# Performance work log

Measured on AMD Instinct MI355X. Metric: run time of the kernel, lower is better.

Reference implementation:

```python
import jax, jax.numpy as jnp
import numpy as np

S, N, D, F, E = 2048, 8, 1024, 4096, 8
STD = 0.02


def setup_inputs() -> dict:
    key = jax.random.key(0)
    ks = jax.random.split(key, 5)
    x = jax.random.normal(ks[0], (S, N, D), dtype=jnp.float32)
    Wg = jax.random.normal(ks[1], (E, D), dtype=jnp.float32) * STD
    W1 = jax.random.normal(ks[2], (E, F, D), dtype=jnp.float32) * STD
    b1 = jnp.zeros((E, F), dtype=jnp.float32)
    W2 = jax.random.normal(ks[3], (E, D, F), dtype=jnp.float32) * STD
    b2 = jnp.zeros((E, D), dtype=jnp.float32)
    return {"x": x, "Wg": Wg, "W1": W1, "b1": b1, "W2": W2, "b2": b2}


def reference(x, Wg, W1, b1, W2, b2):
    # Gate (eval mode: no gating noise). scores: [S, N, E]
    scores = jnp.einsum('snd,ed->sne', x, Wg)
    prob = jax.nn.softmax(scores, axis=-1)
    top1_idx = jnp.argmax(prob, axis=-1)                                   # [S, N] int
    top1_prob = jnp.take_along_axis(prob, top1_idx[..., None], axis=-1)[..., 0]  # [S, N]

    y = jnp.zeros_like(x)
    n_experts = Wg.shape[0]
    for e in range(n_experts):  # small fixed loop over experts
        h = jax.nn.gelu(jnp.einsum('snd,fd->snf', x, W1[e]) + b1[e], approximate=False)
        ye = jnp.einsum('snf,df->snd', h, W2[e]) + b2[e]
        mask = (top1_idx == e)[..., None]                                  # [S, N, 1]
        y = y + jnp.where(mask, ye * top1_prob[..., None], 0.0)
    return y
```

## Files before the change

kernel.cpp:

```cpp
#include <hip/hip_runtime.h>

#define S_TOK 16384
#define D_DIM 1024
#define F_DIM 4096
#define E_NUM 8

#define BM 128
#define BN 128
#define BK 32
#define MT_MAX 136

typedef short bf16x8 __attribute__((ext_vector_type(8)));
typedef float f32x4 __attribute__((ext_vector_type(4)));
typedef unsigned short ushort_t;

static __device__ __forceinline__ unsigned short f32_bf16(float f) {
  unsigned u = __float_as_uint(f);
  return (unsigned short)((u + 0x7FFFu + ((u >> 16) & 1u)) >> 16);
}

static __device__ __forceinline__ unsigned int pack_bf16x2(float a, float b) {
  unsigned ua = __float_as_uint(a);
  unsigned ub = __float_as_uint(b);
  unsigned lo = (ua + 0x7FFFu + ((ua >> 16) & 1u)) >> 16;
  unsigned hi = (ub + 0x7FFFu + ((ub >> 16) & 1u)) & 0xFFFF0000u;
  return lo | hi;
}

static __device__ __forceinline__ uint2 cvt_f4_bf4(const float4 v) {
  uint2 r;
  r.x = pack_bf16x2(v.x, v.y);
  r.y = pack_bf16x2(v.z, v.w);
  return r;
}

static __device__ __forceinline__ void load_lds16(const void* g, void* l) {
  __builtin_amdgcn_global_load_lds(g, l, 16, 0, 0);
}

__global__ void zero_counts_kernel(int* counts) {
  if (threadIdx.x < E_NUM) counts[threadIdx.x] = 0;
}

__global__ void cast2_kernel(const float* __restrict__ w1, ushort_t* __restrict__ o1,
                             const float* __restrict__ w2, ushort_t* __restrict__ o2) {
  const int half = 16384;
  const float* src = (blockIdx.x < half) ? w1 : w2;
  ushort_t* dst = (blockIdx.x < half) ? o1 : o2;
  const int b = (blockIdx.x < half) ? blockIdx.x : (blockIdx.x - half);
  const size_t base = ((size_t)b * blockDim.x + threadIdx.x) * 8;
  const float4 v0 = *(const float4*)(src + base);
  const float4 v1 = *(const float4*)(src + base + 4);
  const uint2 a = cvt_f4_bf4(v0), c = cvt_f4_bf4(v1);
  uint4 w; w.x = a.x; w.y = a.y; w.z = c.x; w.w = c.y;
  *(uint4*)(dst + base) = w;
}

__global__ void gate_kernel(const float* __restrict__ x,
                            const float* __restrict__ Wg,
                            ushort_t* __restrict__ xbf,
                            float* __restrict__ prob,
                            int* __restrict__ counts,
                            int* __restrict__ tok_list) {
  const int wv = threadIdx.x >> 6;
  const int lane = threadIdx.x & 63;
  const int t = blockIdx.x * 4 + wv;
  const float* xr = x + (size_t)t * D_DIM;
  ushort_t* xb = xbf + (size_t)t * D_DIM;

  float acc[E_NUM];
#pragma unroll
  for (int e = 0; e < E_NUM; ++e) acc[e] = 0.0f;

#pragma unroll
  for (int i = 0; i < 4; ++i) {
    const int k = i * 256 + lane * 4;
    const float4 v = *(const float4*)(xr + k);
    *(uint2*)(xb + k) = cvt_f4_bf4(v);
#pragma unroll
    for (int e = 0; e < E_NUM; ++e) {
      const float4 w = *(const float4*)(Wg + e * D_DIM + k);
      acc[e] += v.x * w.x + v.y * w.y + v.z * w.z + v.w * w.w;
    }
  }
#pragma unroll
  for (int e = 0; e < E_NUM; ++e) {
#pragma unroll
    for (int off = 32; off > 0; off >>= 1)
      acc[e] += __shfl_xor(acc[e], off, 64);
  }
  if (lane == 0) {
    float m = acc[0]; int bi = 0;
#pragma unroll
    for (int e = 1; e < E_NUM; ++e) {
      if (acc[e] > m) { m = acc[e]; bi = e; }
    }
    float s = 0.0f;
#pragma unroll
    for (int e = 0; e < E_NUM; ++e) s += expf(acc[e] - m);
    prob[t] = 1.0f / s;
    int p = atomicAdd(&counts[bi], 1);
    tok_list[bi * S_TOK + p] = t;
  }
}

__global__ void plan_kernel(const int* __restrict__ counts, int* __restrict__ plan) {
  if (threadIdx.x == 0) {
    int t = 0;
    for (int e = 0; e < E_NUM; ++e) {
      const int nt = (counts[e] + BM - 1) / BM;
      for (int i = 0; i < nt; ++i) {
        plan[1 + t] = e;
        plan[1 + MT_MAX + t] = i * BM;
        ++t;
      }
    }
    plan[0] = t;
  }
}

template <int KDIM, int NDIM, int EPI>
__launch_bounds__(256, 4)
__global__ void ffn_kernel(const ushort_t* __restrict__ A,
                           const ushort_t* __restrict__ B,
                           const float* __restrict__ bias,
                           const float* __restrict__ prob,
                           const int* __restrict__ counts,
                           const int* __restrict__ tok_list,
                           const int* __restrict__ plan,
                           ushort_t* __restrict__ Hout,
                           float* __restrict__ out) {
  constexpr int NT = NDIM / BN;
  constexpr int NK = KDIM / BK;
  const int ntiles = plan[0];
  const int live = ntiles * NT;
  if (blockIdx.x >= live) return;
  const int q = live >> 3, r = live & 7;
  const int xcd = blockIdx.x & 7, idx = blockIdx.x >> 3;
  const int wg = (xcd < r ? xcd * (q + 1) : r * (q + 1) + (xcd - r) * q) + idx;
  const int tile = wg / NT;
  const int n0 = (wg % NT) * BN;
  const int e = plan[1 + tile];
  const int m0 = plan[1 + MT_MAX + tile];
  const int cnt = counts[e];

  __shared__ ushort_t As[2][BM * BK];
  __shared__ ushort_t Bs[2][BM * BK];

  const int tid = threadIdx.x;
  const int lane = tid & 63;
  const int w = tid >> 6;
  const int wr = (w >> 1) * 64;
  const int wc = (w & 1) * 64;
  const int l15 = lane & 15;
  const int l4  = lane >> 4;

  const int srow = tid >> 2;
  const int sslot = ((tid & 3) ^ ((srow >> 1) & 3)) * 8;
  const int dstoff = w * 512;

  const size_t ebase = (size_t)e * S_TOK;
  const int tokA0 = (m0 + srow < cnt) ? tok_list[ebase + m0 + srow] : 0;
  const int tokA1 = (m0 + 64 + srow < cnt) ? tok_list[ebase + m0 + 64 + srow] : 0;
  const ushort_t* pA0 = A + (size_t)tokA0 * KDIM + sslot;
  const ushort_t* pA1 = A + (size_t)tokA1 * KDIM + sslot;
  const ushort_t* Be = B + (size_t)e * NDIM * KDIM;
  const ushort_t* pB0 = Be + (size_t)(n0 + srow) * KDIM + sslot;
  const ushort_t* pB1 = Be + (size_t)(n0 + 64 + srow) * KDIM + sslot;

  int oA[4], oB[4];
#pragma unroll
  for (int m = 0; m < 4; ++m) {
    const int rr = wr + m * 16 + l15;
    oA[m] = rr * BK + ((l4 ^ ((rr >> 1) & 3)) * 8);
  }
#pragma unroll
  for (int n = 0; n < 4; ++n) {
    const int rr = wc + n * 16 + l15;
    oB[n] = rr * BK + ((l4 ^ ((rr >> 1) & 3)) * 8);
  }

  f32x4 acc[4][4];
#pragma unroll
  for (int i = 0; i < 4; ++i)
#pragma unroll
    for (int j = 0; j < 4; ++j)
      acc[i][j] = (f32x4){0.f, 0.f, 0.f, 0.f};

  load_lds16(pA0, &As[0][dstoff]);
  load_lds16(pA1, &As[0][2048 + dstoff]);
  load_lds16(pB0, &Bs[0][dstoff]);
  load_lds16(pB1, &Bs[0][2048 + dstoff]);
  __syncthreads();

  int cb = 0;
  for (int t = 0; t < NK; ++t) {
    if (t + 1 < NK) {
      const int k0 = (t + 1) * BK;
      const int nb = cb ^ 1;
      load_lds16(pA0 + k0, &As[nb][dstoff]);
      load_lds16(pA1 + k0, &As[nb][2048 + dstoff]);
      load_lds16(pB0 + k0, &Bs[nb][dstoff]);
      load_lds16(pB1 + k0, &Bs[nb][2048 + dstoff]);
    }

    bf16x8 a[4], b[4];
#pragma unroll
    for (int i = 0; i < 4; ++i) {
      a[i] = *(const bf16x8*)&As[cb][oA[i]];
      b[i] = *(const bf16x8*)&Bs[cb][oB[i]];
    }
#pragma unroll
    for (int mi = 0; mi < 4; ++mi)
#pragma unroll
      for (int ni = 0; ni < 4; ++ni)
        acc[mi][ni] = __builtin_amdgcn_mfma_f32_16x16x32_bf16(a[mi], b[ni], acc[mi][ni], 0, 0, 0);

    __syncthreads();
    cb ^= 1;
  }

  const float* be = bias + (size_t)e * NDIM;
#pragma unroll
  for (int mi = 0; mi < 4; ++mi) {
#pragma unroll
    for (int rr = 0; rr < 4; ++rr) {
      const int slot = m0 + wr + mi * 16 + l4 * 4 + rr;
      if (slot >= cnt) continue;
      const int tok = tok_list[ebase + slot];
      if (EPI == 0) {
        ushort_t* hrow = Hout + (size_t)tok * NDIM;
#pragma unroll
        for (int ni = 0; ni < 4; ++ni) {
          const int col = n0 + wc + ni * 16 + l15;
          float v = acc[mi][ni][rr] + be[col];
          v = 0.5f * v * (1.0f + erff(v * 0.70710678118654752f));
          hrow[col] = f32_bf16(v);
        }
      } else {
        const float p = prob[tok];
        float* orow = out + (size_t)tok * NDIM;
#pragma unroll
        for (int ni = 0; ni < 4; ++ni) {
          const int col = n0 + wc + ni * 16 + l15;
          orow[col] = (acc[mi][ni][rr] + be[col]) * p;
        }
      }
    }
  }
}

extern "C" void kernel_launch(void* const* d_in, const int* in_sizes, int n_in,
                              void* d_out, int out_size, void* d_ws, size_t ws_size,
                              hipStream_t stream) {
  const float* x  = (const float*)d_in[0];
  const float* Wg = (const float*)d_in[1];
  const float* W1 = (const float*)d_in[2];
  const float* b1 = (const float*)d_in[3];
  const float* W2 = (const float*)d_in[4];
  const float* b2 = (const float*)d_in[5];
  float* out = (float*)d_out;

  const size_t MB = 1ull << 20;
  char* ws = (char*)d_ws;
  int* counts      = (int*)(ws);
  int* plan        = (int*)(ws + 4096);
  float* prob      = (float*)(ws + 64 * 1024);
  int* tok_list    = (int*)(ws + 128 * 1024);
  ushort_t* xbf    = (ushort_t*)(ws + 1 * MB);
  ushort_t* W1bf   = (ushort_t*)(ws + 33 * MB);
  ushort_t* W2bf   = (ushort_t*)(ws + 97 * MB);
  ushort_t* H      = (ushort_t*)(ws + 161 * MB);

  zero_counts_kernel<<<1, 64, 0, stream>>>(counts);
  gate_kernel<<<S_TOK / 4, 256, 0, stream>>>(x, Wg, xbf, prob, counts, tok_list);
  plan_kernel<<<1, 64, 0, stream>>>(counts, plan);

  cast2_kernel<<<32768, 256, 0, stream>>>(W1, W1bf, W2, W2bf);

  ffn_kernel<D_DIM, F_DIM, 0><<<(F_DIM / BN) * MT_MAX, 256, 0, stream>>>(
      xbf, W1bf, b1, nullptr, counts, tok_list, plan, H, nullptr);

  ffn_kernel<F_DIM, D_DIM, 1><<<(D_DIM / BN) * MT_MAX, 256, 0, stream>>>(
      H, W2bf, b2, prob, counts, tok_list, plan, nullptr, out);
}
```

Measured before the change: 761.2 us.

## Double K tile to 64 and drop LDS double buffering in grouped MoE GEMM

Result: faster. 709.3 us (-6.8%).

```diff
diff --git a/kernel.cpp b/kernel.cpp
--- a/kernel.cpp
+++ b/kernel.cpp
@@ -7,7 +7,7 @@
 
 #define BM 128
 #define BN 128
-#define BK 32
+#define BK 64
 #define MT_MAX 136
 
 typedef short bf16x8 __attribute__((ext_vector_type(8)));
@@ -144,8 +144,8 @@
   const int m0 = plan[1 + MT_MAX + tile];
   const int cnt = counts[e];
 
-  __shared__ ushort_t As[2][BM * BK];
-  __shared__ ushort_t Bs[2][BM * BK];
+  __shared__ ushort_t As[BM * BK];
+  __shared__ ushort_t Bs[BM * BK];
 
   const int tid = threadIdx.x;
   const int lane = tid & 63;
@@ -155,29 +155,36 @@
   const int l15 = lane & 15;
   const int l4  = lane >> 4;
 
-  const int srow = tid >> 2;
-  const int sslot = ((tid & 3) ^ ((srow >> 1) & 3)) * 8;
-  const int dstoff = w * 512;
+  const int sub = lane >> 3;
+  const int sslot = ((lane & 7) ^ sub) * 8;
+  const int dstoff = w * 2048;
 
   const size_t ebase = (size_t)e * S_TOK;
-  const int tokA0 = (m0 + srow < cnt) ? tok_list[ebase + m0 + srow] : 0;
-  const int tokA1 = (m0 + 64 + srow < cnt) ? tok_list[ebase + m0 + 64 + srow] : 0;
-  const ushort_t* pA0 = A + (size_t)tokA0 * KDIM + sslot;
-  const ushort_t* pA1 = A + (size_t)tokA1 * KDIM + sslot;
   const ushort_t* Be = B + (size_t)e * NDIM * KDIM;
-  const ushort_t* pB0 = Be + (size_t)(n0 + srow) * KDIM + sslot;
-  const ushort_t* pB1 = Be + (size_t)(n0 + 64 + srow) * KDIM + sslot;
-
-  int oA[4], oB[4];
+  const ushort_t* pA[4];
+  const ushort_t* pB[4];
+#pragma unroll
+  for (int j = 0; j < 4; ++j) {
+    const int ra = m0 + w * 32 + j * 8 + sub;
+    const int tok = (ra < cnt) ? tok_list[ebase + ra] : 0;
+    pA[j] = A + (size_t)tok * KDIM + sslot;
+    pB[j] = Be + (size_t)(n0 + w * 32 + j * 8 + sub) * KDIM + sslot;
+  }
+
+  int oA[4][2], oB[4][2];
 #pragma unroll
   for (int m = 0; m < 4; ++m) {
     const int rr = wr + m * 16 + l15;
-    oA[m] = rr * BK + ((l4 ^ ((rr >> 1) & 3)) * 8);
+#pragma unroll
+    for (int kk = 0; kk < 2; ++kk)
+      oA[m][kk] = rr * BK + (((kk * 4 + l4) ^ (rr & 7)) * 8);
   }
 #pragma unroll
   for (int n = 0; n < 4; ++n) {
     const int rr = wc + n * 16 + l15;
-    oB[n] = rr * BK + ((l4 ^ ((rr >> 1) & 3)) * 8);
+#pragma unroll
+    for (int kk = 0; kk < 2; ++kk)
+      oB[n][kk] = rr * BK + (((kk * 4 + l4) ^ (rr & 7)) * 8);
   }
 
   f32x4 acc[4][4];
@@ -187,37 +194,31 @@
     for (int j = 0; j < 4; ++j)
       acc[i][j] = (f32x4){0.f, 0.f, 0.f, 0.f};
 
-  load_lds16(pA0, &As[0][dstoff]);
-  load_lds16(pA1, &As[0][2048 + dstoff]);
-  load_lds16(pB0, &Bs[0][dstoff]);
-  load_lds16(pB1, &Bs[0][2048 + dstoff]);
-  __syncthreads();
-
-  int cb = 0;
   for (int t = 0; t < NK; ++t) {
-    if (t + 1 < NK) {
-      const int k0 = (t + 1) * BK;
-      const int nb = cb ^ 1;
-      load_lds16(pA0 + k0, &As[nb][dstoff]);
-      load_lds16(pA1 + k0, &As[nb][2048 + dstoff]);
-      load_lds16(pB0 + k0, &Bs[nb][dstoff]);
-      load_lds16(pB1 + k0, &Bs[nb][2048 + dstoff]);
-    }
-
-    bf16x8 a[4], b[4];
-#pragma unroll
-    for (int i = 0; i < 4; ++i) {
-      a[i] = *(const bf16x8*)&As[cb][oA[i]];
-      b[i] = *(const bf16x8*)&Bs[cb][oB[i]];
-    }
-#pragma unroll
-    for (int mi = 0; mi < 4; ++mi)
-#pragma unroll
-      for (int ni = 0; ni < 4; ++ni)
-        acc[mi][ni] = __builtin_amdgcn_mfma_f32_16x16x32_bf16(a[mi], b[ni], acc[mi][ni], 0, 0, 0);
-
+    const int k0 = t * BK;
+#pragma unroll
+    for (int j = 0; j < 4; ++j) {
+      load_lds16(pA[j] + k0, &As[dstoff + j * 512]);
+      load_lds16(pB[j] + k0, &Bs[dstoff + j * 512]);
+    }
     __syncthreads();
-    cb ^= 1;
+
+#pragma unroll
+    for (int kk = 0; kk < 2; ++kk) {
+      bf16x8 a[4], b[4];
+#pragma unroll
+      for (int i = 0; i < 4; ++i) {
+        a[i] = *(const bf16x8*)&As[oA[i][kk]];
+        b[i] = *(const bf16x8*)&Bs[oB[i][kk]];
+      }
+#pragma unroll
+      for (int mi = 0; mi < 4; ++mi)
+#pragma unroll
+        for (int ni = 0; ni < 4; ++ni)
+          acc[mi][ni] = __builtin_amdgcn_mfma_f32_16x16x32_bf16(a[mi], b[ni], acc[mi][ni], 0, 0, 0);
+    }
+
+    __syncthreads();
   }
 
   const float* be = bias + (size_t)e * NDIM;
```

## Triple-buffer LDS loads with explicit vmcnt waits and reorder tile mapping

Applied to the files above, without the earlier changes.

Result: slower. 790.8 us (+3.9%).

```diff
diff --git a/kernel.cpp b/kernel.cpp
--- a/kernel.cpp
+++ b/kernel.cpp
@@ -36,6 +36,16 @@
 
 static __device__ __forceinline__ void load_lds16(const void* g, void* l) {
   __builtin_amdgcn_global_load_lds(g, l, 16, 0, 0);
+}
+
+static __device__ __forceinline__ float gelu_f(float v) {
+  const float u = fabsf(v) * 0.70710678118654752f;
+  const float t = 1.0f / (1.0f + 0.3275911f * u);
+  const float poly = t * (0.254829592f + t * (-0.284496736f + t * (1.421413741f +
+                     t * (-1.453152027f + t * 1.061405429f))));
+  const float erfa = 1.0f - poly * __expf(-u * u);
+  const float erfv = (v >= 0.0f) ? erfa : -erfa;
+  return 0.5f * v * (1.0f + erfv);
 }
 
 __global__ void zero_counts_kernel(int* counts) {
@@ -119,8 +129,10 @@
   }
 }
 
+#define SWZ(r) ((((r) & 3) ^ (((r) >> 2) & 3)))
+
 template <int KDIM, int NDIM, int EPI>
-__launch_bounds__(256, 4)
+__launch_bounds__(256, 3)
 __global__ void ffn_kernel(const ushort_t* __restrict__ A,
                            const ushort_t* __restrict__ B,
                            const float* __restrict__ bias,
@@ -138,14 +150,14 @@
   const int q = live >> 3, r = live & 7;
   const int xcd = blockIdx.x & 7, idx = blockIdx.x >> 3;
   const int wg = (xcd < r ? xcd * (q + 1) : r * (q + 1) + (xcd - r) * q) + idx;
-  const int tile = wg / NT;
-  const int n0 = (wg % NT) * BN;
+  const int tile = wg % ntiles;
+  const int n0 = (wg / ntiles) * BN;
   const int e = plan[1 + tile];
   const int m0 = plan[1 + MT_MAX + tile];
   const int cnt = counts[e];
 
-  __shared__ ushort_t As[2][BM * BK];
-  __shared__ ushort_t Bs[2][BM * BK];
+  __shared__ ushort_t As[3][BM * BK];
+  __shared__ ushort_t Bs[3][BM * BK];
 
   const int tid = threadIdx.x;
   const int lane = tid & 63;
@@ -156,8 +168,8 @@
   const int l4  = lane >> 4;
 
   const int srow = tid >> 2;
-  const int sslot = ((tid & 3) ^ ((srow >> 1) & 3)) * 8;
-  const int dstoff = w * 512;
+  const int sslot = ((tid & 3) ^ SWZ(srow)) * 8;
+  const int w512 = w * 512;
 
   const size_t ebase = (size_t)e * S_TOK;
   const int tokA0 = (m0 + srow < cnt) ? tok_list[ebase + m0 + srow] : 0;
@@ -172,12 +184,12 @@
 #pragma unroll
   for (int m = 0; m < 4; ++m) {
     const int rr = wr + m * 16 + l15;
-    oA[m] = rr * BK + ((l4 ^ ((rr >> 1) & 3)) * 8);
+    oA[m] = rr * BK + ((l4 ^ SWZ(rr)) * 8);
   }
 #pragma unroll
   for (int n = 0; n < 4; ++n) {
     const int rr = wc + n * 16 + l15;
-    oB[n] = rr * BK + ((l4 ^ ((rr >> 1) & 3)) * 8);
+    oB[n] = rr * BK + ((l4 ^ SWZ(rr)) * 8);
   }
 
   f32x4 acc[4][4];
@@ -187,22 +199,20 @@
     for (int j = 0; j < 4; ++j)
       acc[i][j] = (f32x4){0.f, 0.f, 0.f, 0.f};
 
-  load_lds16(pA0, &As[0][dstoff]);
-  load_lds16(pA1, &As[0][2048 + dstoff]);
-  load_lds16(pB0, &Bs[0][dstoff]);
-  load_lds16(pB1, &Bs[0][2048 + dstoff]);
-  __syncthreads();
+#pragma unroll
+  for (int p = 0; p < 3; ++p) {
+    const int k0 = p * BK;
+    load_lds16(pA0 + k0, &As[p][w512]);
+    load_lds16(pA1 + k0, &As[p][2048 + w512]);
+    load_lds16(pB0 + k0, &Bs[p][w512]);
+    load_lds16(pB1 + k0, &Bs[p][2048 + w512]);
+  }
 
   int cb = 0;
   for (int t = 0; t < NK; ++t) {
-    if (t + 1 < NK) {
-      const int k0 = (t + 1) * BK;
-      const int nb = cb ^ 1;
-      load_lds16(pA0 + k0, &As[nb][dstoff]);
-      load_lds16(pA1 + k0, &As[nb][2048 + dstoff]);
-      load_lds16(pB0 + k0, &Bs[nb][dstoff]);
-      load_lds16(pB1 + k0, &Bs[nb][2048 + dstoff]);
-    }
+    asm volatile("s_waitcnt vmcnt(8)" ::: "memory");
+    __builtin_amdgcn_s_barrier();
+    __builtin_amdgcn_sched_barrier(0);
 
     bf16x8 a[4], b[4];
 #pragma unroll
@@ -216,8 +226,16 @@
       for (int ni = 0; ni < 4; ++ni)
         acc[mi][ni] = __builtin_amdgcn_mfma_f32_16x16x32_bf16(a[mi], b[ni], acc[mi][ni], 0, 0, 0);
 
-    __syncthreads();
-    cb ^= 1;
+    __builtin_amdgcn_sched_barrier(0);
+    __builtin_amdgcn_s_barrier();
+
+    const int kst = ((t + 3 < NK) ? (t + 3) : (NK - 1)) * BK;
+    load_lds16(pA0 + kst, &As[cb][w512]);
+    load_lds16(pA1 + kst, &As[cb][2048 + w512]);
+    load_lds16(pB0 + kst, &Bs[cb][w512]);
+    load_lds16(pB1 + kst, &Bs[cb][2048 + w512]);
+
+    cb = (cb == 2) ? 0 : cb + 1;
   }
 
   const float* be = bias + (size_t)e * NDIM;
@@ -233,9 +251,7 @@
 #pragma unroll
         for (int ni = 0; ni < 4; ++ni) {
           const int col = n0 + wc + ni * 16 + l15;
-          float v = acc[mi][ni][rr] + be[col];
-          v = 0.5f * v * (1.0f + erff(v * 0.70710678118654752f));
-          hrow[col] = f32_bf16(v);
+          hrow[col] = f32_bf16(gelu_f(acc[mi][ni][rr] + be[col]));
         }
       } else {
         const float p = prob[tok];
```
